# Kernel optimization log

Hardware: AMD Instinct MI355X
Metric: run time of the kernel (lower is better)

## Reference

```python
import jax, jax.numpy as jnp
import numpy as np

MARGIN = jnp.float32(0.0)


def setup_inputs() -> dict:
    key = jax.random.key(0)
    k1, k2 = jax.random.split(key)
    cos_pred = jax.random.uniform(k1, (4096, 8192), dtype=jnp.float32)
    mask_gt = jax.random.randint(k2, (4096, 8192), 0, 2, dtype=jnp.int32)
    return {"cos_pred": cos_pred, "mask_gt": mask_gt}


def reference(cos_pred, mask_gt):
    # RankerEmbLoss with rank_type == 'avg', margin == 0.0, fully vectorized:
    # per row i: mean over gt entries of (1 - cos), mean over non-gt entries of
    # relu(cos - margin); then average means over rows.
    mask = mask_gt.astype(bool)                      # [n_docs, n_qs]
    n_qs = cos_pred.shape[1]
    cnt_t = jnp.sum(mask, axis=1).astype(cos_pred.dtype)          # positives per row
    cnt_nt = (n_qs - cnt_t).astype(cos_pred.dtype)                # negatives per row
    sum_t = jnp.sum(jnp.where(mask, 1.0 - cos_pred, 0.0), axis=1)
    sum_nt = jnp.sum(jnp.where(mask, 0.0, jnp.maximum(cos_pred - MARGIN, 0.0)), axis=1)
    loss_tgt = jnp.mean(sum_t / cnt_t)
    loss_nontgt = jnp.mean(sum_nt / cnt_nt)
    loss = (loss_tgt + loss_nontgt) * 0.5
    return (loss, loss_tgt, loss_nontgt)
```

## Files before the change

### kernel.cpp

```cpp
#include <hip/hip_runtime.h>

constexpr int N_DOCS = 4096;
constexpr int N_QS   = 8192;
constexpr int BLOCK  = 256;
constexpr int WAVES_PER_BLOCK = BLOCK / 64;
constexpr int GRID  = N_DOCS / WAVES_PER_BLOCK;
constexpr int VECS_PER_ROW = N_QS / 4;
constexpr int VECS_PER_LANE = VECS_PER_ROW / 64;
constexpr int CHUNK = 8;
constexpr int N_CHUNKS = VECS_PER_LANE / CHUNK;

typedef float fx4 __attribute__((ext_vector_type(4)));
typedef int   ix4 __attribute__((ext_vector_type(4)));

__global__ __launch_bounds__(BLOCK) void row_reduce_kernel(
    const fx4* __restrict__ cos4,
    const ix4* __restrict__ mask4,
    float2* __restrict__ row_out)
{
    const int tid  = threadIdx.x;
    const int lane = tid & 63;
    const int row  = blockIdx.x * WAVES_PER_BLOCK + (tid >> 6);
    const long base = (long)row * VECS_PER_ROW + lane;

    float s_mc = 0.f, s_nt = 0.f;
    int   icnt = 0;

#pragma unroll
    for (int ch = 0; ch < N_CHUNKS; ++ch) {
        fx4 c[CHUNK];
        ix4 m[CHUNK];
#pragma unroll
        for (int v = 0; v < CHUNK; ++v) {
            const long idx = base + (long)(ch * CHUNK + v) * 64;
            c[v] = __builtin_nontemporal_load(&cos4[idx]);
            m[v] = __builtin_nontemporal_load(&mask4[idx]);
        }
#pragma unroll
        for (int v = 0; v < CHUNK; ++v) {
            s_mc += (m[v].x != 0) ? c[v].x : 0.f;
            s_mc += (m[v].y != 0) ? c[v].y : 0.f;
            s_mc += (m[v].z != 0) ? c[v].z : 0.f;
            s_mc += (m[v].w != 0) ? c[v].w : 0.f;

            s_nt += (m[v].x != 0) ? 0.f : fmaxf(c[v].x, 0.f);
            s_nt += (m[v].y != 0) ? 0.f : fmaxf(c[v].y, 0.f);
            s_nt += (m[v].z != 0) ? 0.f : fmaxf(c[v].z, 0.f);
            s_nt += (m[v].w != 0) ? 0.f : fmaxf(c[v].w, 0.f);

            icnt += m[v].x + m[v].y + m[v].z + m[v].w;
        }
    }

    float cf = (float)icnt;
#pragma unroll
    for (int off = 32; off > 0; off >>= 1) {
        s_mc += __shfl_down(s_mc, off);
        s_nt += __shfl_down(s_nt, off);
        cf   += __shfl_down(cf,   off);
    }

    if (lane == 0) {
        float t      = cf - s_mc;
        float cnt_nt = (float)N_QS - cf;
        row_out[row] = make_float2(t / cf, s_nt / cnt_nt);
    }
}

__global__ __launch_bounds__(1024) void final_reduce_kernel(
    const float2* __restrict__ row_out,
    float* __restrict__ out)
{
    const int tid = threadIdx.x;
    float a = 0.f, b = 0.f;
#pragma unroll
    for (int i = tid; i < N_DOCS; i += 1024) {
        float2 r = row_out[i];
        a += r.x;
        b += r.y;
    }
#pragma unroll
    for (int off = 32; off > 0; off >>= 1) {
        a += __shfl_down(a, off);
        b += __shfl_down(b, off);
    }
    __shared__ float sa[16], sb[16];
    const int wave = tid >> 6;
    const int lane = tid & 63;
    if (lane == 0) { sa[wave] = a; sb[wave] = b; }
    __syncthreads();
    if (tid == 0) {
        float ta = 0.f, tb = 0.f;
#pragma unroll
        for (int w = 0; w < 16; ++w) { ta += sa[w]; tb += sb[w]; }
        float loss_tgt    = ta / (float)N_DOCS;
        float loss_nontgt = tb / (float)N_DOCS;
        out[0] = (loss_tgt + loss_nontgt) * 0.5f;
        out[1] = loss_tgt;
        out[2] = loss_nontgt;
    }
}

extern "C" void kernel_launch(void* const* d_in, const int* in_sizes, int n_in,
                              void* d_out, int out_size, void* d_ws, size_t ws_size,
                              hipStream_t stream) {
    const fx4* cos4  = (const fx4*)d_in[0];
    const ix4* mask4 = (const ix4*)d_in[1];
    float2* row_out = (float2*)d_ws;
    float*  out     = (float*)d_out;

    row_reduce_kernel<<<GRID, BLOCK, 0, stream>>>(cos4, mask4, row_out);
    final_reduce_kernel<<<1, 1024, 0, stream>>>(row_out, out);
}
```

Baseline: 249.4 us.

## Split each row across two waves and combine partial sums in final reduce

Each row is now handled by two waves that each reduce half the columns, which doubles the grid to 2048 blocks. The per-row division moves into the final kernel, which adds the two partial float4 results per row. The load chunk shrinks from 8 to 4, and launch bounds request 8 blocks per CU to raise occupancy and memory-level parallelism. The cost is a larger partial buffer and a little more work in the single-block final reduction.

```diff
diff --git a/kernel.cpp b/kernel.cpp
--- a/kernel.cpp
+++ b/kernel.cpp
@@ -3,25 +3,26 @@
 constexpr int N_DOCS = 4096;
 constexpr int N_QS   = 8192;
 constexpr int BLOCK  = 256;
-constexpr int WAVES_PER_BLOCK = BLOCK / 64;
-constexpr int GRID  = N_DOCS / WAVES_PER_BLOCK;
-constexpr int VECS_PER_ROW = N_QS / 4;
-constexpr int VECS_PER_LANE = VECS_PER_ROW / 64;
-constexpr int CHUNK = 8;
+constexpr int SPLITS = 2;
+constexpr int N_PART = N_DOCS * SPLITS;
+constexpr int GRID   = N_PART / (BLOCK / 64);
+constexpr int HALF_VECS = (N_QS / SPLITS) / 4;
+constexpr int VECS_PER_LANE = HALF_VECS / 64;
+constexpr int CHUNK = 4;
 constexpr int N_CHUNKS = VECS_PER_LANE / CHUNK;
 
 typedef float fx4 __attribute__((ext_vector_type(4)));
 typedef int   ix4 __attribute__((ext_vector_type(4)));
 
-__global__ __launch_bounds__(BLOCK) void row_reduce_kernel(
+__global__ __launch_bounds__(BLOCK, 8) void row_reduce_kernel(
     const fx4* __restrict__ cos4,
     const ix4* __restrict__ mask4,
-    float2* __restrict__ row_out)
+    float4* __restrict__ partial)
 {
     const int tid  = threadIdx.x;
     const int lane = tid & 63;
-    const int row  = blockIdx.x * WAVES_PER_BLOCK + (tid >> 6);
-    const long base = (long)row * VECS_PER_ROW + lane;
+    const int part = blockIdx.x * (BLOCK / 64) + (tid >> 6);
+    const long base = (long)part * HALF_VECS + lane;
 
     float s_mc = 0.f, s_nt = 0.f;
     int   icnt = 0;
@@ -60,24 +61,25 @@
         cf   += __shfl_down(cf,   off);
     }
 
-    if (lane == 0) {
-        float t      = cf - s_mc;
-        float cnt_nt = (float)N_QS - cf;
-        row_out[row] = make_float2(t / cf, s_nt / cnt_nt);
-    }
+    if (lane == 0)
+        partial[part] = make_float4(s_mc, s_nt, cf, 0.f);
 }
 
 __global__ __launch_bounds__(1024) void final_reduce_kernel(
-    const float2* __restrict__ row_out,
+    const float4* __restrict__ partial,
     float* __restrict__ out)
 {
     const int tid = threadIdx.x;
     float a = 0.f, b = 0.f;
 #pragma unroll
-    for (int i = tid; i < N_DOCS; i += 1024) {
-        float2 r = row_out[i];
-        a += r.x;
-        b += r.y;
+    for (int r = tid; r < N_DOCS; r += 1024) {
+        float4 p0 = partial[2 * r];
+        float4 p1 = partial[2 * r + 1];
+        float mc = p0.x + p1.x;
+        float nt = p0.y + p1.y;
+        float ct = p0.z + p1.z;
+        a += (ct - mc) / ct;
+        b += nt / ((float)N_QS - ct);
     }
 #pragma unroll
     for (int off = 32; off > 0; off >>= 1) {
@@ -106,9 +108,9 @@
                               hipStream_t stream) {
     const fx4* cos4  = (const fx4*)d_in[0];
     const ix4* mask4 = (const ix4*)d_in[1];
-    float2* row_out = (float2*)d_ws;
+    float4* partial = (float4*)d_ws;
     float*  out     = (float*)d_out;
 
-    row_reduce_kernel<<<GRID, BLOCK, 0, stream>>>(cos4, mask4, row_out);
-    final_reduce_kernel<<<1, 1024, 0, stream>>>(row_out, out);
+    row_reduce_kernel<<<GRID, BLOCK, 0, stream>>>(cos4, mask4, partial);
+    final_reduce_kernel<<<1, 1024, 0, stream>>>(partial, out);
 }
```

Result: no change. 250.8 us (+0.6%).
